# Kernel tuning notes

Hardware: AMD Instinct MI355X
Metric: run time of the kernel (lower is better)

## Reference

```python
import jax, jax.numpy as jnp
import numpy as np

D_MODEL = 1024
NUM_HEADS = 16
HEAD_DIM = D_MODEL // NUM_HEADS
D_FF = 4096
LN_EPS = 1e-6  # flax nnx.LayerNorm default


def setup_inputs() -> dict:
    key = jax.random.key(0)
    ks = jax.random.split(key, 13)
    s_in = 1.0 / np.sqrt(D_MODEL)
    s_ff = 1.0 / np.sqrt(D_FF)
    return {
        "x": jax.random.normal(ks[0], (2, 2048, D_MODEL), dtype=jnp.float32),
        "Wq": jax.random.normal(ks[1], (D_MODEL, D_MODEL), jnp.float32) * s_in,
        "bq": jnp.zeros((D_MODEL,), jnp.float32),
        "Wk": jax.random.normal(ks[2], (D_MODEL, D_MODEL), jnp.float32) * s_in,
        "bk": jnp.zeros((D_MODEL,), jnp.float32),
        "Wv": jax.random.normal(ks[3], (D_MODEL, D_MODEL), jnp.float32) * s_in,
        "bv": jnp.zeros((D_MODEL,), jnp.float32),
        "Wo": jax.random.normal(ks[4], (D_MODEL, D_MODEL), jnp.float32) * s_in,
        "bo": jnp.zeros((D_MODEL,), jnp.float32),
        "W1": jax.random.normal(ks[5], (D_MODEL, D_FF), jnp.float32) * s_in,
        "b1": jnp.zeros((D_FF,), jnp.float32),
        "W2": jax.random.normal(ks[6], (D_FF, D_MODEL), jnp.float32) * s_ff,
        "b2": jnp.zeros((D_MODEL,), jnp.float32),
        "ln1_scale": jnp.ones((D_MODEL,), jnp.float32),
        "ln1_bias": jnp.zeros((D_MODEL,), jnp.float32),
        "ln2_scale": jnp.ones((D_MODEL,), jnp.float32),
        "ln2_bias": jnp.zeros((D_MODEL,), jnp.float32),
    }


def layer_norm(x, scale, bias):
    mu = jnp.mean(x, axis=-1, keepdims=True)
    var = jnp.mean(jnp.square(x - mu), axis=-1, keepdims=True)
    return (x - mu) * jax.lax.rsqrt(var + LN_EPS) * scale + bias


def reference(x, Wq, bq, Wk, bk, Wv, bv, Wo, bo, W1, b1, W2, b2,
              ln1_scale, ln1_bias, ln2_scale, ln2_bias):
    B, S, _ = x.shape
    h = layer_norm(x, ln1_scale, ln1_bias)
    # project and split heads: [B, H, S, Dh]
    q = (h @ Wq + bq).reshape(B, S, NUM_HEADS, HEAD_DIM).transpose(0, 2, 1, 3)
    k = (h @ Wk + bk).reshape(B, S, NUM_HEADS, HEAD_DIM).transpose(0, 2, 1, 3)
    v = (h @ Wv + bv).reshape(B, S, NUM_HEADS, HEAD_DIM).transpose(0, 2, 1, 3)
    scores = jnp.einsum("bhqd,bhkd->bhqk", q, k) / jnp.sqrt(jnp.float32(HEAD_DIM))
    attn = jax.nn.softmax(scores, axis=-1)
    out = jnp.einsum("bhqk,bhkd->bhqd", attn, v)
    out = out.transpose(0, 2, 1, 3).reshape(B, S, D_MODEL)
    x = x + out @ Wo + bo
    h2 = layer_norm(x, ln2_scale, ln2_bias)
    ff = jax.nn.relu(h2 @ W1 + b1) @ W2 + b2
    return x + ff
```

## Files before the change

### kernel.cpp

```cpp
#include <hip/hip_runtime.h>

typedef unsigned short ushort_t;
typedef __attribute__((ext_vector_type(8))) __bf16 bf16x8;
typedef __attribute__((ext_vector_type(8))) unsigned short ushort8v;
typedef __attribute__((ext_vector_type(4))) float floatx4;

__device__ inline float b2f(ushort_t u) {
    union { unsigned int i; float f; } c; c.i = ((unsigned int)u) << 16; return c.f;
}
__device__ inline ushort_t f2b(float f) {
    union { float f; unsigned int i; } c; c.f = f;
    unsigned int i = c.i;
    unsigned int r = (i + 0x7FFFu + ((i >> 16) & 1u)) >> 16;
    return (ushort_t)r;
}
__device__ inline bf16x8 as_bf16x8(ushort8v u) { return __builtin_bit_cast(bf16x8, u); }

__global__ __launch_bounds__(256) void concat3_kernel(
    const float* __restrict__ a, const float* __restrict__ b,
    const float* __restrict__ c, float* __restrict__ o) {
    int t = blockIdx.x * 256 + threadIdx.x;
    if (t < 3072)
        o[t] = t < 1024 ? a[t] : (t < 2048 ? b[t - 1024] : c[t - 2048]);
}

__global__ __launch_bounds__(256) void transpose_conv_kernel(
    const float* __restrict__ in, ushort_t* __restrict__ out,
    int R, int Csub, int ldin) {
    __shared__ float tile[32][33];
    int tx = threadIdx.x, ty = threadIdx.y;
    int r0 = blockIdx.y * 32, c0 = blockIdx.x * 32;
#pragma unroll
    for (int i = 0; i < 32; i += 8)
        tile[ty + i][tx] = in[(size_t)(r0 + ty + i) * ldin + c0 + tx];
    __syncthreads();
#pragma unroll
    for (int i = 0; i < 32; i += 8)
        out[(size_t)(c0 + ty + i) * R + r0 + tx] = f2b(tile[tx][ty + i]);
}

__global__ __launch_bounds__(256) void transpose_v_kernel(
    const ushort_t* __restrict__ qkv, ushort_t* __restrict__ vt) {
    __shared__ ushort_t tile[32][33];
    int tx = threadIdx.x, ty = threadIdx.y;
    int s0 = blockIdx.x * 32, d0 = blockIdx.y * 32;
    int bh = blockIdx.z, b = bh >> 4, h = bh & 15;
    const ushort_t* src = qkv + (size_t)b * 2048 * 3072 + 2048 + h * 64;
    ushort_t* dst = vt + (size_t)bh * 64 * 2048;
#pragma unroll
    for (int i = 0; i < 32; i += 8)
        tile[ty + i][tx] = src[(size_t)(s0 + ty + i) * 3072 + d0 + tx];
    __syncthreads();
#pragma unroll
    for (int i = 0; i < 32; i += 8)
        dst[(size_t)(d0 + ty + i) * 2048 + s0 + tx] = tile[tx][ty + i];
}

__device__ inline float wave_sum(float s) {
#pragma unroll
    for (int o = 32; o > 0; o >>= 1) s += __shfl_xor(s, o);
    return s;
}

__global__ __launch_bounds__(256) void ln_f32_kernel(
    const float* __restrict__ x, const float* __restrict__ sc,
    const float* __restrict__ bi, ushort_t* __restrict__ out) {
    int row = blockIdx.x, t = threadIdx.x;
    const float* xr = x + (size_t)row * 1024;
    float4 u = *(const float4*)(xr + t * 4);
    float v0 = u.x, v1 = u.y, v2 = u.z, v3 = u.w;
    __shared__ float sm[8];
    int wv = t >> 6, lane = t & 63;
    float s = wave_sum(v0 + v1 + v2 + v3);
    if (lane == 0) sm[wv] = s;
    __syncthreads();
    float mean = (sm[0] + sm[1] + sm[2] + sm[3]) * (1.0f / 1024.0f);
    float d0 = v0 - mean, d1 = v1 - mean, d2 = v2 - mean, d3 = v3 - mean;
    float q = wave_sum(d0 * d0 + d1 * d1 + d2 * d2 + d3 * d3);
    if (lane == 0) sm[4 + wv] = q;
    __syncthreads();
    float var = (sm[4] + sm[5] + sm[6] + sm[7]) * (1.0f / 1024.0f);
    float rn = rsqrtf(var + 1e-6f);
    float4 us = *(const float4*)(sc + t * 4);
    float4 ub = *(const float4*)(bi + t * 4);
    ushort4 o;
    o.x = f2b(d0 * rn * us.x + ub.x);
    o.y = f2b(d1 * rn * us.y + ub.y);
    o.z = f2b(d2 * rn * us.z + ub.z);
    o.w = f2b(d3 * rn * us.w + ub.w);
    *(ushort4*)(out + (size_t)row * 1024 + t * 4) = o;
}

__global__ __launch_bounds__(256) void gemm_bt_kernel(
    const ushort_t* __restrict__ A, const ushort_t* __restrict__ Bt,
    const float* __restrict__ bias, const float* __restrict__ resf,
    ushort_t* __restrict__ Cb, float* __restrict__ Cf,
    int M, int N, int K, int ldb, int op) {
    __shared__ __align__(16) ushort_t As[128 * 40];
    __shared__ __align__(16) ushort_t Bs[128 * 40];
    int tid = threadIdx.x;
    int m0 = blockIdx.y * 128, n0 = blockIdx.x * 128;
    int wv = tid >> 6, lane = tid & 63;
    int wr = wv & 1, wc = wv >> 1;
    int mo = wr * 64, no = wc * 64;
    int quad = lane >> 4, l16 = lane & 15;
    int k8 = quad * 8;

    floatx4 acc[4][4] = {};

    for (int k0 = 0; k0 < K; k0 += 32) {
#pragma unroll
        for (int c = 0; c < 2; ++c) {
            int e = c * 2048 + tid * 8;
            int r = e >> 5, kk = e & 31;
            *(ushort8v*)(As + r * 40 + kk) = *(const ushort8v*)(A + (size_t)(m0 + r) * K + k0 + kk);
            *(ushort8v*)(Bs + r * 40 + kk) = *(const ushort8v*)(Bt + (size_t)(n0 + r) * ldb + k0 + kk);
        }
        __syncthreads();
        bf16x8 af[4], bfr[4];
#pragma unroll
        for (int i = 0; i < 4; ++i) {
            af[i]  = as_bf16x8(*(const ushort8v*)(As + (mo + i * 16 + l16) * 40 + k8));
            bfr[i] = as_bf16x8(*(const ushort8v*)(Bs + (no + i * 16 + l16) * 40 + k8));
        }
#pragma unroll
        for (int mi = 0; mi < 4; ++mi)
#pragma unroll
            for (int ni = 0; ni < 4; ++ni)
                acc[mi][ni] = __builtin_amdgcn_mfma_f32_16x16x32_bf16(
                    af[mi], bfr[ni], acc[mi][ni], 0, 0, 0);
        __syncthreads();
    }

#pragma unroll
    for (int mi = 0; mi < 4; ++mi) {
#pragma unroll
        for (int r = 0; r < 4; ++r) {
            int row = m0 + mo + mi * 16 + quad * 4 + r;
            size_t rowoff = (size_t)row * N;
#pragma unroll
            for (int ni = 0; ni < 4; ++ni) {
                int col = n0 + no + ni * 16 + l16;
                float val = acc[mi][ni][r];
                if (op != 3) val += bias[col];
                if (op == 1) val = fmaxf(val, 0.0f);
                if (op >= 2) {
                    val += resf[rowoff + col];
                    Cf[rowoff + col] = val;
                } else {
                    Cb[rowoff + col] = f2b(val);
                }
            }
        }
    }
}

__global__ __launch_bounds__(256) void attn_kernel(
    const ushort_t* __restrict__ qkv, const ushort_t* __restrict__ vt,
    ushort_t* __restrict__ om) {
    const int LDQ = 3072, LDO = 1024;
    int bh = blockIdx.y;
    int b = bh >> 4, h = bh & 15;
    size_t qbase = (size_t)b * 2048 * LDQ + h * 64;
    size_t kbase = qbase + 1024;
    const ushort_t* vtp = vt + (size_t)bh * 64 * 2048;
    int q0 = blockIdx.x * 128;
    int tid = threadIdx.x, wv = tid >> 6, lane = tid & 63;
    int quad = lane >> 4, l16 = lane & 15;
    int k8 = quad * 8;

    __shared__ __align__(16) ushort_t Ks[64 * 72];
    __shared__ __align__(16) ushort_t Vs[64 * 72];
    __shared__ __align__(16) ushort_t Ps[4 * 32 * 76];
    ushort_t* ps = Ps + wv * 32 * 76;

    int sr0 = tid >> 3, scc0 = (tid & 7) * 8;
    int sr1 = sr0 + 32;

    bf16x8 qf[2][2];
#pragma unroll
    for (int mt = 0; mt < 2; ++mt) {
        const ushort_t* qptr = qkv + qbase + (size_t)(q0 + wv * 32 + mt * 16 + l16) * LDQ;
        qf[mt][0] = as_bf16x8(*(const ushort8v*)(qptr + k8));
        qf[mt][1] = as_bf16x8(*(const ushort8v*)(qptr + 32 + k8));
    }

    bf16x8 ones;
#pragma unroll
    for (int j = 0; j < 8; ++j) ones[j] = (__bf16)1.0f;

    floatx4 Oacc[2][4] = {};
    floatx4 lsum[2] = {};

    ushort8v kreg0, kreg1, vreg0, vreg1;
    kreg0 = *(const ushort8v*)(qkv + kbase + (size_t)sr0 * LDQ + scc0);
    kreg1 = *(const ushort8v*)(qkv + kbase + (size_t)sr1 * LDQ + scc0);
    vreg0 = *(const ushort8v*)(vtp + (size_t)sr0 * 2048 + scc0);
    vreg1 = *(const ushort8v*)(vtp + (size_t)sr1 * 2048 + scc0);

    for (int kb = 0; kb < 2048; kb += 64) {
        __syncthreads();
        *(ushort8v*)(Ks + sr0 * 72 + scc0) = kreg0;
        *(ushort8v*)(Ks + sr1 * 72 + scc0) = kreg1;
        *(ushort8v*)(Vs + sr0 * 72 + scc0) = vreg0;
        *(ushort8v*)(Vs + sr1 * 72 + scc0) = vreg1;
        __syncthreads();

        int nkb = (kb + 64 < 2048) ? kb + 64 : 0;
        kreg0 = *(const ushort8v*)(qkv + kbase + (size_t)(nkb + sr0) * LDQ + scc0);
        kreg1 = *(const ushort8v*)(qkv + kbase + (size_t)(nkb + sr1) * LDQ + scc0);
        vreg0 = *(const ushort8v*)(vtp + (size_t)sr0 * 2048 + nkb + scc0);
        vreg1 = *(const ushort8v*)(vtp + (size_t)sr1 * 2048 + nkb + scc0);

        bf16x8 kf[4][2];
#pragma unroll
        for (int kt = 0; kt < 4; ++kt)
#pragma unroll
            for (int ds = 0; ds < 2; ++ds)
                kf[kt][ds] = as_bf16x8(
                    *(const ushort8v*)(Ks + (kt * 16 + l16) * 72 + ds * 32 + k8));

        floatx4 sc[2][4];
#pragma unroll
        for (int mt = 0; mt < 2; ++mt)
#pragma unroll
            for (int kt = 0; kt < 4; ++kt) {
                floatx4 s = {0.0f, 0.0f, 0.0f, 0.0f};
                s = __builtin_amdgcn_mfma_f32_16x16x32_bf16(qf[mt][0], kf[kt][0], s, 0, 0, 0);
                s = __builtin_amdgcn_mfma_f32_16x16x32_bf16(qf[mt][1], kf[kt][1], s, 0, 0, 0);
                sc[mt][kt] = s;
            }

#pragma unroll
        for (int mt = 0; mt < 2; ++mt)
#pragma unroll
            for (int kt = 0; kt < 4; ++kt)
#pragma unroll
                for (int r = 0; r < 4; ++r)
                    ps[(mt * 16 + quad * 4 + r) * 76 + kt * 16 + l16] =
                        f2b(__expf(sc[mt][kt][r] * 0.125f));

        bf16x8 vf[4][2];
#pragma unroll
        for (int dt = 0; dt < 4; ++dt)
#pragma unroll
            for (int ks = 0; ks < 2; ++ks)
                vf[dt][ks] = as_bf16x8(
                    *(const ushort8v*)(Vs + (dt * 16 + l16) * 72 + ks * 32 + k8));
#pragma unroll
        for (int mt = 0; mt < 2; ++mt) {
            bf16x8 pf0 = as_bf16x8(*(const ushort8v*)(ps + (mt * 16 + l16) * 76 + k8));
            bf16x8 pf1 = as_bf16x8(*(const ushort8v*)(ps + (mt * 16 + l16) * 76 + 32 + k8));
#pragma unroll
            for (int dt = 0; dt < 4; ++dt) {
                Oacc[mt][dt] = __builtin_amdgcn_mfma_f32_16x16x32_bf16(pf0, vf[dt][0], Oacc[mt][dt], 0, 0, 0);
                Oacc[mt][dt] = __builtin_amdgcn_mfma_f32_16x16x32_bf16(pf1, vf[dt][1], Oacc[mt][dt], 0, 0, 0);
            }
            lsum[mt] = __builtin_amdgcn_mfma_f32_16x16x32_bf16(pf0, ones, lsum[mt], 0, 0, 0);
            lsum[mt] = __builtin_amdgcn_mfma_f32_16x16x32_bf16(pf1, ones, lsum[mt], 0, 0, 0);
        }
    }

#pragma unroll
    for (int mt = 0; mt < 2; ++mt)
#pragma unroll
        for (int r = 0; r < 4; ++r) {
            float inv = 1.0f / lsum[mt][r];
            size_t rowoff = (size_t)(b * 2048 + q0 + wv * 32 + mt * 16 + quad * 4 + r) * LDO + h * 64;
#pragma unroll
            for (int dt = 0; dt < 4; ++dt)
                om[rowoff + dt * 16 + l16] = f2b(Oacc[mt][dt][r] * inv);
        }
}

extern "C" void kernel_launch(void* const* d_in, const int* in_sizes, int n_in,
                              void* d_out, int out_size, void* d_ws, size_t ws_size,
                              hipStream_t stream) {
    const float* x    = (const float*)d_in[0];
    const float* Wq   = (const float*)d_in[1];
    const float* bq   = (const float*)d_in[2];
    const float* Wk   = (const float*)d_in[3];
    const float* bk   = (const float*)d_in[4];
    const float* Wv   = (const float*)d_in[5];
    const float* bv   = (const float*)d_in[6];
    const float* Wo   = (const float*)d_in[7];
    const float* bo   = (const float*)d_in[8];
    const float* W1   = (const float*)d_in[9];
    const float* b1   = (const float*)d_in[10];
    const float* W2   = (const float*)d_in[11];
    const float* b2   = (const float*)d_in[12];
    const float* ln1s = (const float*)d_in[13];
    const float* ln1b = (const float*)d_in[14];
    const float* ln2s = (const float*)d_in[15];
    const float* ln2b = (const float*)d_in[16];
    float*    outf = (float*)d_out;
    ushort_t* ws   = (ushort_t*)d_ws;

    const size_t M1 = 1048576;
    ushort_t* qkvT    = ws;
    ushort_t* WoT     = ws + 3 * M1;
    ushort_t* W1T     = ws + 4 * M1;
    ushort_t* W2T     = ws + 8 * M1;
    ushort_t* h       = ws + 12 * M1;
    ushort_t* attnout = ws + 12 * M1;
    ushort_t* qkv     = ws + 16 * M1;
    ushort_t* h2      = ws + 16 * M1;
    ushort_t* ffc     = ws + 20 * M1;
    float*    bqkv    = (float*)(ws + 28 * M1);
    ushort_t* vtbuf   = (ushort_t*)d_out;

    dim3 tb(32, 8);
    dim3 tg(32, 32);

    concat3_kernel<<<12, 256, 0, stream>>>(bq, bk, bv, bqkv);
    transpose_conv_kernel<<<tg, tb, 0, stream>>>(Wq, qkvT,           1024, 1024, 1024);
    transpose_conv_kernel<<<tg, tb, 0, stream>>>(Wk, qkvT + 1 * M1,  1024, 1024, 1024);
    transpose_conv_kernel<<<tg, tb, 0, stream>>>(Wv, qkvT + 2 * M1,  1024, 1024, 1024);
    transpose_conv_kernel<<<tg, tb, 0, stream>>>(Wo, WoT,            1024, 1024, 1024);
    transpose_conv_kernel<<<dim3(128, 32), tb, 0, stream>>>(W1, W1T, 1024, 4096, 4096);
    transpose_conv_kernel<<<dim3(32, 128), tb, 0, stream>>>(W2, W2T, 4096, 1024, 1024);

    ln_f32_kernel<<<4096, 256, 0, stream>>>(x, ln1s, ln1b, h);

    gemm_bt_kernel<<<dim3(24, 32), 256, 0, stream>>>(
        h, qkvT, bqkv, nullptr, qkv, nullptr, 4096, 3072, 1024, 1024, 0);

    transpose_v_kernel<<<dim3(64, 2, 32), tb, 0, stream>>>(qkv, vtbuf);

    attn_kernel<<<dim3(16, 32), 256, 0, stream>>>(qkv, vtbuf, attnout);

    gemm_bt_kernel<<<dim3(8, 32), 256, 0, stream>>>(
        attnout, WoT, bo, x, nullptr, outf, 4096, 1024, 1024, 1024, 2);

    ln_f32_kernel<<<4096, 256, 0, stream>>>(outf, ln2s, ln2b, h2);

    for (int c = 0; c < 2; ++c) {
        gemm_bt_kernel<<<dim3(16, 32), 256, 0, stream>>>(
            h2, W1T + (size_t)c * 2048 * 1024, b1 + c * 2048, nullptr,
            ffc, nullptr, 4096, 2048, 1024, 1024, 1);
        gemm_bt_kernel<<<dim3(8, 32), 256, 0, stream>>>(
            ffc, W2T + (size_t)c * 2048, b2, outf,
            nullptr, outf, 4096, 1024, 2048, 4096, c == 0 ? 2 : 3);
    }
}
```

Baseline: 571.8 us.

## Split-K with atomic accumulation for Wo and W2 GEMMs, merge FFN chunks

```diff
diff --git a/kernel.cpp b/kernel.cpp
--- a/kernel.cpp
+++ b/kernel.cpp
@@ -22,6 +22,12 @@
     int t = blockIdx.x * 256 + threadIdx.x;
     if (t < 3072)
         o[t] = t < 1024 ? a[t] : (t < 2048 ? b[t - 1024] : c[t - 2048]);
+}
+
+__global__ __launch_bounds__(256) void copy_f32_kernel(
+    const float* __restrict__ src, float* __restrict__ dst) {
+    size_t i = ((size_t)blockIdx.x * 256 + threadIdx.x) * 4;
+    *(float4*)(dst + i) = *(const float4*)(src + i);
 }
 
 __global__ __launch_bounds__(256) void transpose_conv_kernel(
@@ -155,6 +161,65 @@
     }
 }
 
+__global__ __launch_bounds__(256) void gemm_bt_atomic_kernel(
+    const ushort_t* __restrict__ A, const ushort_t* __restrict__ Bt,
+    const float* __restrict__ bias, float* __restrict__ Cf,
+    int M, int N, int lda, int ldb, int Kc) {
+    __shared__ __align__(16) ushort_t As[128 * 40];
+    __shared__ __align__(16) ushort_t Bs[128 * 40];
+    int tid = threadIdx.x;
+    int m0 = blockIdx.y * 128, n0 = blockIdx.x * 128;
+    int kbase = blockIdx.z * Kc;
+    int wv = tid >> 6, lane = tid & 63;
+    int wr = wv & 1, wc = wv >> 1;
+    int mo = wr * 64, no = wc * 64;
+    int quad = lane >> 4, l16 = lane & 15;
+    int k8 = quad * 8;
+
+    floatx4 acc[4][4] = {};
+
+    for (int k0 = kbase; k0 < kbase + Kc; k0 += 32) {
+#pragma unroll
+        for (int c = 0; c < 2; ++c) {
+            int e = c * 2048 + tid * 8;
+            int r = e >> 5, kk = e & 31;
+            *(ushort8v*)(As + r * 40 + kk) = *(const ushort8v*)(A + (size_t)(m0 + r) * lda + k0 + kk);
+            *(ushort8v*)(Bs + r * 40 + kk) = *(const ushort8v*)(Bt + (size_t)(n0 + r) * ldb + k0 + kk);
+        }
+        __syncthreads();
+        bf16x8 af[4], bfr[4];
+#pragma unroll
+        for (int i = 0; i < 4; ++i) {
+            af[i]  = as_bf16x8(*(const ushort8v*)(As + (mo + i * 16 + l16) * 40 + k8));
+            bfr[i] = as_bf16x8(*(const ushort8v*)(Bs + (no + i * 16 + l16) * 40 + k8));
+        }
+#pragma unroll
+        for (int mi = 0; mi < 4; ++mi)
+#pragma unroll
+            for (int ni = 0; ni < 4; ++ni)
+                acc[mi][ni] = __builtin_amdgcn_mfma_f32_16x16x32_bf16(
+                    af[mi], bfr[ni], acc[mi][ni], 0, 0, 0);
+        __syncthreads();
+    }
+
+    bool addb = (blockIdx.z == 0) && (bias != nullptr);
+#pragma unroll
+    for (int mi = 0; mi < 4; ++mi) {
+#pragma unroll
+        for (int r = 0; r < 4; ++r) {
+            int row = m0 + mo + mi * 16 + quad * 4 + r;
+            size_t rowoff = (size_t)row * N;
+#pragma unroll
+            for (int ni = 0; ni < 4; ++ni) {
+                int col = n0 + no + ni * 16 + l16;
+                float val = acc[mi][ni][r];
+                if (addb) val += bias[col];
+                unsafeAtomicAdd(&Cf[rowoff + col], val);
+            }
+        }
+    }
+}
+
 __global__ __launch_bounds__(256) void attn_kernel(
     const ushort_t* __restrict__ qkv, const ushort_t* __restrict__ vt,
     ushort_t* __restrict__ om) {
@@ -304,9 +369,9 @@
     ushort_t* h       = ws + 12 * M1;
     ushort_t* attnout = ws + 12 * M1;
     ushort_t* qkv     = ws + 16 * M1;
-    ushort_t* h2      = ws + 16 * M1;
-    ushort_t* ffc     = ws + 20 * M1;
-    float*    bqkv    = (float*)(ws + 28 * M1);
+    ushort_t* h2      = ws;
+    ushort_t* ffbuf   = ws + 12 * M1;
+    float*    bqkv    = (float*)d_out;
     ushort_t* vtbuf   = (ushort_t*)d_out;
 
     dim3 tb(32, 8);
@@ -329,17 +394,15 @@
 
     attn_kernel<<<dim3(16, 32), 256, 0, stream>>>(qkv, vtbuf, attnout);
 
-    gemm_bt_kernel<<<dim3(8, 32), 256, 0, stream>>>(
-        attnout, WoT, bo, x, nullptr, outf, 4096, 1024, 1024, 1024, 2);
+    copy_f32_kernel<<<4096, 256, 0, stream>>>(x, outf);
+    gemm_bt_atomic_kernel<<<dim3(8, 32, 4), 256, 0, stream>>>(
+        attnout, WoT, bo, outf, 4096, 1024, 1024, 1024, 256);
 
     ln_f32_kernel<<<4096, 256, 0, stream>>>(outf, ln2s, ln2b, h2);
 
-    for (int c = 0; c < 2; ++c) {
-        gemm_bt_kernel<<<dim3(16, 32), 256, 0, stream>>>(
-            h2, W1T + (size_t)c * 2048 * 1024, b1 + c * 2048, nullptr,
-            ffc, nullptr, 4096, 2048, 1024, 1024, 1);
-        gemm_bt_kernel<<<dim3(8, 32), 256, 0, stream>>>(
-            ffc, W2T + (size_t)c * 2048, b2, outf,
-            nullptr, outf, 4096, 1024, 2048, 4096, c == 0 ? 2 : 3);
-    }
-}
+    gemm_bt_kernel<<<dim3(32, 32), 256, 0, stream>>>(
+        h2, W1T, b1, nullptr, ffbuf, nullptr, 4096, 4096, 1024, 1024, 1);
+
+    gemm_bt_atomic_kernel<<<dim3(8, 32, 4), 256, 0, stream>>>(
+        ffbuf, W2T, b2, outf, 4096, 1024, 4096, 4096, 1024);
+}
```

Result: faster. 538.7 us (-5.8%).
